# Kernel optimization log

Measured on AMD Instinct MI355X. Metric: run time of the kernel, lower is better.

The kernel has to match this reference:

```python
import jax, jax.numpy as jnp
import numpy as np


def setup_inputs() -> dict:
    key = jax.random.key(0)
    ks = jax.random.split(key, 8)
    B, T, U = 4, 400, 80
    De, Dd, V = 512, 512, 1024
    F = De + Dd  # in_features = 1024
    s = lambda k, shape: jax.random.normal(k, shape, dtype=jnp.float32) * 0.05
    return {
        "encoder_output": jax.random.normal(ks[0], (B, T, De), dtype=jnp.float32),
        "decoder_output": jax.random.normal(ks[1], (B, U, Dd), dtype=jnp.float32),
        "W_enc": s(ks[2], (F, De)),
        "b_enc": s(ks[3], (F,)),
        "W_dec": s(ks[4], (F, Dd)),
        "b_dec": s(ks[5], (F,)),
        "W_fc": s(ks[6], (V, F)),
        "b_fc": s(ks[7], (V,)),
    }


def reference(encoder_output, decoder_output, W_enc, b_enc, W_dec, b_dec, W_fc, b_fc):
    # fc_enc / fc_dec projections: (B,T,F) and (B,U,F)
    enc = jnp.einsum("btd,fd->btf", encoder_output, W_enc) + b_enc
    dec = jnp.einsum("bud,fd->buf", decoder_output, W_dec) + b_dec
    # broadcast-add -> (B,T,U,F)
    combined = enc[:, :, None, :] + dec[:, None, :, :]
    # fc: tanh then linear -> (B,T,U,V)
    vocab_logits = jnp.einsum("btuf,vf->btuv", jnp.tanh(combined), W_fc) + b_fc
    # HAT branch: blank prob via sigmoid of logit 0
    blk_logit = vocab_logits[..., :1]
    log_blk = jax.nn.log_sigmoid(blk_logit)          # log(sigmoid)
    log_not_blk = jax.nn.log_sigmoid(-blk_logit)     # log(1 - sigmoid)
    vocab_log_probs = log_not_blk + jax.nn.log_softmax(vocab_logits[..., 1:], axis=-1)
    return jnp.concatenate([log_blk, vocab_log_probs], axis=-1)
```

## Files before the change

### kernel.cpp

```cpp
#include <hip/hip_runtime.h>
#include <hip/hip_bf16.h>
#include <cstdint>
#include <cstddef>

typedef short bf16x8 __attribute__((ext_vector_type(8)));
typedef float f32x4 __attribute__((ext_vector_type(4)));

static __device__ __forceinline__ unsigned short f2bf(float f) {
    union { float f; uint32_t u; } c; c.f = f;
    uint32_t r = c.u + 0x7FFFu + ((c.u >> 16) & 1u);
    return (unsigned short)(r >> 16);
}

static __device__ __forceinline__ float fast_tanh(float x) {
    float e = __expf(2.0f * x);
    return 1.0f - 2.0f / (e + 1.0f);
}

static __device__ __forceinline__ float softplus_f(float x) {
    return fmaxf(x, 0.0f) + log1pf(__expf(-fabsf(x)));
}

__global__ __launch_bounds__(256) void k_convert(
    const float* __restrict__ s0, const float* __restrict__ s1,
    const float* __restrict__ s2, const float* __restrict__ s3,
    const float* __restrict__ s4,
    unsigned short* __restrict__ d0, unsigned short* __restrict__ d1,
    unsigned short* __restrict__ d2, unsigned short* __restrict__ d3,
    unsigned short* __restrict__ d4,
    int n0, int n1, int n2, int n3, int n4)
{
    int i = blockIdx.x * 256 + threadIdx.x;
    int c0 = n0 >> 2, c1 = c0 + (n1 >> 2), c2 = c1 + (n2 >> 2),
        c3 = c2 + (n3 >> 2), c4 = c3 + (n4 >> 2);
    if (i >= c4) return;
    const float* s; unsigned short* d; int j;
    if (i < c0)      { s = s0; d = d0; j = i; }
    else if (i < c1) { s = s1; d = d1; j = i - c0; }
    else if (i < c2) { s = s2; d = d2; j = i - c1; }
    else if (i < c3) { s = s3; d = d3; j = i - c2; }
    else             { s = s4; d = d4; j = i - c3; }
    float4 v = reinterpret_cast<const float4*>(s)[j];
    ushort4 o;
    o.x = f2bf(v.x); o.y = f2bf(v.y); o.z = f2bf(v.z); o.w = f2bf(v.w);
    reinterpret_cast<ushort4*>(d)[j] = o;
}

__global__ __launch_bounds__(256) void k_proj(
    const unsigned short* __restrict__ A,
    const unsigned short* __restrict__ W,
    const float* __restrict__ bias,
    float* __restrict__ out)
{
    __shared__ unsigned short As[32 * 512];
    const int tid = threadIdx.x;
    const int m0 = blockIdx.x * 32;
    const int c0 = blockIdx.y * 128;
    {
        int row = tid >> 3;
        const unsigned short* src = A + (size_t)(m0 + row) * 512;
        unsigned int base = row * 1024;
        unsigned int sw = (row & 7) << 4;
        #pragma unroll
        for (int c = 0; c < 8; ++c) {
            int col = (tid & 7) * 8 + c * 64;
            bf16x8 v = *reinterpret_cast<const bf16x8*>(src + col);
            *reinterpret_cast<bf16x8*>(
                reinterpret_cast<char*>(As) + ((base + col * 2) ^ sw)) = v;
        }
    }
    __syncthreads();
    const int w = tid >> 6, l = tid & 63;
    const int lr = l & 15, lkb = (l >> 4) * 8;
    f32x4 acc[2][2] = {};
    const int colbase = c0 + w * 32;
    const unsigned short* Wb = W + (size_t)(colbase + lr) * 512 + lkb;
    const unsigned int sw = (lr & 7) << 4;
    for (int ks = 0; ks < 16; ++ks) {
        unsigned int kb = (ks * 32 + lkb) * 2;
        bf16x8 a0 = *reinterpret_cast<const bf16x8*>(
            reinterpret_cast<const char*>(As) + ((lr * 1024 + kb) ^ sw));
        bf16x8 a1 = *reinterpret_cast<const bf16x8*>(
            reinterpret_cast<const char*>(As) + (((16 + lr) * 1024 + kb) ^ sw));
        #pragma unroll
        for (int nf = 0; nf < 2; ++nf) {
            bf16x8 b = *reinterpret_cast<const bf16x8*>(Wb + nf * 16 * 512 + ks * 32);
            acc[0][nf] = __builtin_amdgcn_mfma_f32_16x16x32_bf16(a0, b, acc[0][nf], 0, 0, 0);
            acc[1][nf] = __builtin_amdgcn_mfma_f32_16x16x32_bf16(a1, b, acc[1][nf], 0, 0, 0);
        }
    }
    const int qr = (l >> 4) * 4;
    #pragma unroll
    for (int nf = 0; nf < 2; ++nf) {
        int col = colbase + nf * 16 + lr;
        float bv = bias[col];
        #pragma unroll
        for (int mf = 0; mf < 2; ++mf)
            #pragma unroll
            for (int r = 0; r < 4; ++r)
                out[(size_t)(m0 + mf * 16 + qr + r) * 1024 + col] = acc[mf][nf][r] + bv;
    }
}

__global__ __launch_bounds__(512, 2) void k_main(
    const float* __restrict__ enc,
    const float* __restrict__ dec,
    const unsigned short* __restrict__ Wfc,
    const float* __restrict__ bfc,
    float* __restrict__ out)
{
    extern __shared__ char smem[];
    char* As   = smem;
    float* red  = (float*)(smem + 131072);
    float* l0sh = (float*)(smem + 133120);

    const int tid = threadIdx.x;
    const int w = tid >> 6, l = tid & 63;
    const int lr = l & 15, q = l >> 4;
    const int r0 = blockIdx.x * 64;

    {
        int row = tid >> 3, kc = tid & 7;
        int m = r0 + row;
        int bt = m / 80;
        int u  = m - bt * 80;
        int b  = bt / 400;
        const float* ep = enc + (size_t)bt * 1024 + kc * 8;
        const float* dp = dec + (size_t)(b * 80 + u) * 1024 + kc * 8;
        unsigned base = row * 2048 + kc * 16;
        unsigned sw = (row & 7) << 4;
        #pragma unroll
        for (int c = 0; c < 16; ++c) {
            float4 e0 = *(const float4*)(ep + c * 64);
            float4 e1 = *(const float4*)(ep + c * 64 + 4);
            float4 f0 = *(const float4*)(dp + c * 64);
            float4 f1 = *(const float4*)(dp + c * 64 + 4);
            union { unsigned short h[8]; bf16x8 v; } pk;
            pk.h[0] = f2bf(fast_tanh(e0.x + f0.x));
            pk.h[1] = f2bf(fast_tanh(e0.y + f0.y));
            pk.h[2] = f2bf(fast_tanh(e0.z + f0.z));
            pk.h[3] = f2bf(fast_tanh(e0.w + f0.w));
            pk.h[4] = f2bf(fast_tanh(e1.x + f1.x));
            pk.h[5] = f2bf(fast_tanh(e1.y + f1.y));
            pk.h[6] = f2bf(fast_tanh(e1.z + f1.z));
            pk.h[7] = f2bf(fast_tanh(e1.w + f1.w));
            *(bf16x8*)(As + ((base + c * 128) ^ sw)) = pk.v;
        }
    }
    __syncthreads();

    const unsigned short* Wb = Wfc + (size_t)(w * 128 + lr) * 1024 + q * 8;
    const unsigned sw = (lr & 7) << 4;

    f32x4 acc[4][8] = {};
    bf16x8 B0[8], B1[8];

    #pragma unroll
    for (int nf = 0; nf < 8; ++nf)
        B0[nf] = *(const bf16x8*)(Wb + nf * 16384);
    #pragma unroll
    for (int nf = 0; nf < 8; ++nf)
        B1[nf] = *(const bf16x8*)(Wb + nf * 16384 + 32);

    #pragma unroll
    for (int kp = 0; kp < 16; ++kp) {
        const int ks0 = 2 * kp, ks1 = 2 * kp + 1;
        {
            bf16x8 a[4];
            #pragma unroll
            for (int mf = 0; mf < 4; ++mf)
                a[mf] = *(const bf16x8*)(As +
                    (((unsigned)(lr * 2048 + mf * 32768 + q * 16 + ks0 * 64)) ^ sw));
            #pragma unroll
            for (int nf = 0; nf < 8; ++nf) {
                #pragma unroll
                for (int mf = 0; mf < 4; ++mf)
                    acc[mf][nf] = __builtin_amdgcn_mfma_f32_16x16x32_bf16(
                        a[mf], B0[nf], acc[mf][nf], 0, 0, 0);
                if (ks0 + 2 < 32)
                    B0[nf] = *(const bf16x8*)(Wb + nf * 16384 + (ks0 + 2) * 32);
            }
        }
        {
            bf16x8 a[4];
            #pragma unroll
            for (int mf = 0; mf < 4; ++mf)
                a[mf] = *(const bf16x8*)(As +
                    (((unsigned)(lr * 2048 + mf * 32768 + q * 16 + ks1 * 64)) ^ sw));
            #pragma unroll
            for (int nf = 0; nf < 8; ++nf) {
                #pragma unroll
                for (int mf = 0; mf < 4; ++mf)
                    acc[mf][nf] = __builtin_amdgcn_mfma_f32_16x16x32_bf16(
                        a[mf], B1[nf], acc[mf][nf], 0, 0, 0);
                if (ks1 + 2 < 32)
                    B1[nf] = *(const bf16x8*)(Wb + nf * 16384 + (ks1 + 2) * 32);
            }
        }
    }

    #pragma unroll
    for (int nf = 0; nf < 8; ++nf) {
        float bv = bfc[w * 128 + nf * 16 + lr];
        #pragma unroll
        for (int mf = 0; mf < 4; ++mf)
            #pragma unroll
            for (int r = 0; r < 4; ++r)
                acc[mf][nf][r] += bv;
    }
    const bool excl = (w == 0 && lr == 0);
    if (excl) {
        #pragma unroll
        for (int mf = 0; mf < 4; ++mf)
            #pragma unroll
            for (int r = 0; r < 4; ++r)
                l0sh[mf * 16 + q * 4 + r] = acc[mf][0][r];
    }
    float Mrow[4][4];
    #pragma unroll
    for (int mf = 0; mf < 4; ++mf)
        #pragma unroll
        for (int r = 0; r < 4; ++r) {
            float m = -3.0e38f;
            #pragma unroll
            for (int nf = 0; nf < 8; ++nf)
                if (!(excl && nf == 0)) m = fmaxf(m, acc[mf][nf][r]);
            #pragma unroll
            for (int s = 1; s < 16; s <<= 1)
                m = fmaxf(m, __shfl_xor(m, s, 16));
            if (lr == 0) red[(mf * 16 + q * 4 + r) * 8 + w] = m;
        }
    __syncthreads();
    #pragma unroll
    for (int mf = 0; mf < 4; ++mf)
        #pragma unroll
        for (int r = 0; r < 4; ++r) {
            int row = mf * 16 + q * 4 + r;
            float m = red[row * 8 + 0];
            #pragma unroll
            for (int j = 1; j < 8; ++j) m = fmaxf(m, red[row * 8 + j]);
            Mrow[mf][r] = m;
        }
    __syncthreads();
    #pragma unroll
    for (int mf = 0; mf < 4; ++mf)
        #pragma unroll
        for (int r = 0; r < 4; ++r) {
            float s = 0.0f;
            #pragma unroll
            for (int nf = 0; nf < 8; ++nf)
                if (!(excl && nf == 0)) s += __expf(acc[mf][nf][r] - Mrow[mf][r]);
            #pragma unroll
            for (int sh = 1; sh < 16; sh <<= 1)
                s += __shfl_xor(s, sh, 16);
            if (lr == 0) red[(mf * 16 + q * 4 + r) * 8 + w] = s;
        }
    __syncthreads();
    #pragma unroll
    for (int mf = 0; mf < 4; ++mf)
        #pragma unroll
        for (int r = 0; r < 4; ++r) {
            int row = mf * 16 + q * 4 + r;
            float s = red[row * 8 + 0];
            #pragma unroll
            for (int j = 1; j < 8; ++j) s += red[row * 8 + j];
            float lse = Mrow[mf][r] + __logf(s);
            float l0 = l0sh[row];
            float lnb = -softplus_f(l0);
            float* op = out + (size_t)(r0 + row) * 1024;
            #pragma unroll
            for (int nf = 0; nf < 8; ++nf) {
                int col = w * 128 + nf * 16 + lr;
                float val = (col == 0) ? (-softplus_f(-l0))
                                       : (acc[mf][nf][r] - lse + lnb);
                op[col] = val;
            }
        }
}

extern "C" void kernel_launch(void* const* d_in, const int* in_sizes, int n_in,
                              void* d_out, int out_size, void* d_ws, size_t ws_size,
                              hipStream_t stream)
{
    const float* encoder = (const float*)d_in[0];
    const float* decoder = (const float*)d_in[1];
    const float* W_enc   = (const float*)d_in[2];
    const float* b_enc   = (const float*)d_in[3];
    const float* W_dec   = (const float*)d_in[4];
    const float* b_dec   = (const float*)d_in[5];
    const float* W_fc    = (const float*)d_in[6];
    const float* b_fc    = (const float*)d_in[7];
    float* out = (float*)d_out;

    char* ws = (char*)d_ws;
    float*          enc_f  = (float*)(ws);
    float*          dec_f  = (float*)(ws + 6553600);
    unsigned short* Wfc_h  = (unsigned short*)(ws + 7864320);
    unsigned short* Wenc_h = (unsigned short*)(ws + 9961472);
    unsigned short* Wdec_h = (unsigned short*)(ws + 11010048);
    unsigned short* encI_h = (unsigned short*)(ws + 12058624);
    unsigned short* decI_h = (unsigned short*)(ws + 13697024);

    const int nEnc = 4 * 400 * 512, nDec = 4 * 80 * 512;
    const int nWe = 1024 * 512, nWd = 1024 * 512, nWf = 1024 * 1024;
    const int totalF4 = (nEnc + nDec + nWe + nWd + nWf) >> 2;
    k_convert<<<(totalF4 + 255) / 256, 256, 0, stream>>>(
        encoder, decoder, W_enc, W_dec, W_fc,
        encI_h, decI_h, Wenc_h, Wdec_h, Wfc_h,
        nEnc, nDec, nWe, nWd, nWf);

    k_proj<<<dim3(1600 / 32, 8), 256, 0, stream>>>(encI_h, Wenc_h, b_enc, enc_f);
    k_proj<<<dim3(320 / 32, 8), 256, 0, stream>>>(decI_h, Wdec_h, b_dec, dec_f);

    const int SMEM_BYTES = 133376;
    hipFuncSetAttribute(reinterpret_cast<const void*>(k_main),
                        hipFuncAttributeMaxDynamicSharedMemorySize, SMEM_BYTES);
    k_main<<<2000, 512, SMEM_BYTES, stream>>>(enc_f, dec_f, Wfc_h, b_fc, out);
}
```

Baseline: 786.8 us.

## Use 128-row tiles with 1024 threads, splitting vocab and K into halves

```diff
diff --git a/kernel.cpp b/kernel.cpp
--- a/kernel.cpp
+++ b/kernel.cpp
@@ -11,12 +11,16 @@
     uint32_t r = c.u + 0x7FFFu + ((c.u >> 16) & 1u);
     return (unsigned short)(r >> 16);
 }
-
+static __device__ __forceinline__ float bf2f_lo(uint32_t w) {
+    union { uint32_t u; float f; } c; c.u = w << 16; return c.f;
+}
+static __device__ __forceinline__ float bf2f_hi(uint32_t w) {
+    union { uint32_t u; float f; } c; c.u = w & 0xffff0000u; return c.f;
+}
 static __device__ __forceinline__ float fast_tanh(float x) {
     float e = __expf(2.0f * x);
     return 1.0f - 2.0f / (e + 1.0f);
 }
-
 static __device__ __forceinline__ float softplus_f(float x) {
     return fmaxf(x, 0.0f) + log1pf(__expf(-fabsf(x)));
 }
@@ -102,7 +106,7 @@
     }
 }
 
-__global__ __launch_bounds__(512, 2) void k_main(
+__global__ __launch_bounds__(1024, 4) void k_main(
     const float* __restrict__ enc,
     const float* __restrict__ dec,
     const unsigned short* __restrict__ Wfc,
@@ -110,172 +114,234 @@
     float* __restrict__ out)
 {
     extern __shared__ char smem[];
-    char* As   = smem;
+    char*  As   = smem;
     float* red  = (float*)(smem + 131072);
-    float* l0sh = (float*)(smem + 133120);
+    float* Mc   = (float*)(smem + 135168);
+    float* fin  = (float*)(smem + 135680);
+    float* f0sh = (float*)(smem + 136192);
+    float* l0sh = (float*)(smem + 136704);
 
     const int tid = threadIdx.x;
     const int w = tid >> 6, l = tid & 63;
     const int lr = l & 15, q = l >> 4;
-    const int r0 = blockIdx.x * 64;
-
+    const int wm = w >> 3, wn = w & 7;
+
+    const int bid = (int)blockIdx.x;
+    const int sbid = (bid & 7) * 125 + (bid >> 3);
+    const int r0 = sbid * 128;
+
+    const int arow = tid >> 3, akc = tid & 7;
+    const float *ep, *dp;
     {
-        int row = tid >> 3, kc = tid & 7;
-        int m = r0 + row;
+        int m = r0 + arow;
         int bt = m / 80;
-        int u  = m - bt * 80;
-        int b  = bt / 400;
-        const float* ep = enc + (size_t)bt * 1024 + kc * 8;
-        const float* dp = dec + (size_t)(b * 80 + u) * 1024 + kc * 8;
-        unsigned base = row * 2048 + kc * 16;
-        unsigned sw = (row & 7) << 4;
-        #pragma unroll
-        for (int c = 0; c < 16; ++c) {
-            float4 e0 = *(const float4*)(ep + c * 64);
-            float4 e1 = *(const float4*)(ep + c * 64 + 4);
-            float4 f0 = *(const float4*)(dp + c * 64);
-            float4 f1 = *(const float4*)(dp + c * 64 + 4);
-            union { unsigned short h[8]; bf16x8 v; } pk;
-            pk.h[0] = f2bf(fast_tanh(e0.x + f0.x));
-            pk.h[1] = f2bf(fast_tanh(e0.y + f0.y));
-            pk.h[2] = f2bf(fast_tanh(e0.z + f0.z));
-            pk.h[3] = f2bf(fast_tanh(e0.w + f0.w));
-            pk.h[4] = f2bf(fast_tanh(e1.x + f1.x));
-            pk.h[5] = f2bf(fast_tanh(e1.y + f1.y));
-            pk.h[6] = f2bf(fast_tanh(e1.z + f1.z));
-            pk.h[7] = f2bf(fast_tanh(e1.w + f1.w));
-            *(bf16x8*)(As + ((base + c * 128) ^ sw)) = pk.v;
+        int u = m - bt * 80;
+        int b = bt / 400;
+        ep = enc + (size_t)bt * 1024 + akc * 8;
+        dp = dec + (size_t)(b * 80 + u) * 1024 + akc * 8;
+    }
+    const unsigned awbase = (unsigned)(arow * 1024 + akc * 16);
+    const unsigned awkey  = (unsigned)((arow & 7) << 4);
+
+    const unsigned abase = (unsigned)((wm * 64 + lr) * 1024 + q * 16);
+    const unsigned akey  = (unsigned)((lr & 7) << 4);
+
+    char* stash = (char*)(out + (size_t)r0 * 1024 + 512) + w * 8192 + l * 16;
+
+    #pragma unroll
+    for (int vp = 0; vp < 2; ++vp) {
+        const unsigned short* Wv =
+            Wfc + (size_t)(vp * 512 + wn * 64 + lr) * 1024 + q * 8;
+        f32x4 acc[4][4] = {};
+        bf16x8 Bp0[4], Bp1[4];
+        #pragma unroll
+        for (int nf = 0; nf < 4; ++nf) Bp0[nf] = *(const bf16x8*)(Wv + nf * 16384);
+        #pragma unroll
+        for (int nf = 0; nf < 4; ++nf) Bp1[nf] = *(const bf16x8*)(Wv + nf * 16384 + 32);
+
+        #pragma unroll
+        for (int kh = 0; kh < 2; ++kh) {
+            __syncthreads();
+            {
+                const float* eph = ep + kh * 512;
+                const float* dph = dp + kh * 512;
+                #pragma unroll
+                for (int c = 0; c < 8; ++c) {
+                    float4 e0 = *(const float4*)(eph + c * 64);
+                    float4 e1 = *(const float4*)(eph + c * 64 + 4);
+                    float4 f0 = *(const float4*)(dph + c * 64);
+                    float4 f1 = *(const float4*)(dph + c * 64 + 4);
+                    union { unsigned short h[8]; bf16x8 v; } pk;
+                    pk.h[0] = f2bf(fast_tanh(e0.x + f0.x));
+                    pk.h[1] = f2bf(fast_tanh(e0.y + f0.y));
+                    pk.h[2] = f2bf(fast_tanh(e0.z + f0.z));
+                    pk.h[3] = f2bf(fast_tanh(e0.w + f0.w));
+                    pk.h[4] = f2bf(fast_tanh(e1.x + f1.x));
+                    pk.h[5] = f2bf(fast_tanh(e1.y + f1.y));
+                    pk.h[6] = f2bf(fast_tanh(e1.z + f1.z));
+                    pk.h[7] = f2bf(fast_tanh(e1.w + f1.w));
+                    *(bf16x8*)(As + ((awbase + c * 128) ^ awkey)) = pk.v;
+                }
+            }
+            __syncthreads();
+            #pragma unroll
+            for (int kp = 0; kp < 8; ++kp) {
+                {
+                    const int ks = kp * 2, gks = kh * 16 + ks;
+                    bf16x8 a[4];
+                    unsigned ao = (abase + ks * 64) ^ akey;
+                    #pragma unroll
+                    for (int mf = 0; mf < 4; ++mf)
+                        a[mf] = *(const bf16x8*)(As + ao + mf * 16384);
+                    #pragma unroll
+                    for (int nf = 0; nf < 4; ++nf) {
+                        #pragma unroll
+                        for (int mf = 0; mf < 4; ++mf)
+                            acc[mf][nf] = __builtin_amdgcn_mfma_f32_16x16x32_bf16(
+                                a[mf], Bp0[nf], acc[mf][nf], 0, 0, 0);
+                        if (gks + 2 < 32)
+                            Bp0[nf] = *(const bf16x8*)(Wv + nf * 16384 + (gks + 2) * 32);
+                    }
+                }
+                {
+                    const int ks = kp * 2 + 1, gks = kh * 16 + ks;
+                    bf16x8 a[4];
+                    unsigned ao = (abase + ks * 64) ^ akey;
+                    #pragma unroll
+                    for (int mf = 0; mf < 4; ++mf)
+                        a[mf] = *(const bf16x8*)(As + ao + mf * 16384);
+                    #pragma unroll
+                    for (int nf = 0; nf < 4; ++nf) {
+                        #pragma unroll
+                        for (int mf = 0; mf < 4; ++mf)
+                            acc[mf][nf] = __builtin_amdgcn_mfma_f32_16x16x32_bf16(
+                                a[mf], Bp1[nf], acc[mf][nf], 0, 0, 0);
+                        if (gks + 2 < 32)
+                            Bp1[nf] = *(const bf16x8*)(Wv + nf * 16384 + (gks + 2) * 32);
+                    }
+                }
+            }
         }
-    }
-    __syncthreads();
-
-    const unsigned short* Wb = Wfc + (size_t)(w * 128 + lr) * 1024 + q * 8;
-    const unsigned sw = (lr & 7) << 4;
-
-    f32x4 acc[4][8] = {};
-    bf16x8 B0[8], B1[8];
-
-    #pragma unroll
-    for (int nf = 0; nf < 8; ++nf)
-        B0[nf] = *(const bf16x8*)(Wb + nf * 16384);
-    #pragma unroll
-    for (int nf = 0; nf < 8; ++nf)
-        B1[nf] = *(const bf16x8*)(Wb + nf * 16384 + 32);
-
-    #pragma unroll
-    for (int kp = 0; kp < 16; ++kp) {
-        const int ks0 = 2 * kp, ks1 = 2 * kp + 1;
-        {
-            bf16x8 a[4];
+
+        if (vp == 0) {
+            #pragma unroll
+            for (int nf = 0; nf < 4; ++nf) {
+                float bv = bfc[wn * 64 + nf * 16 + lr];
+                #pragma unroll
+                for (int mf = 0; mf < 4; ++mf)
+                    #pragma unroll
+                    for (int r = 0; r < 4; ++r)
+                        acc[mf][nf][r] += bv;
+            }
+            uint32_t wds[32];
             #pragma unroll
             for (int mf = 0; mf < 4; ++mf)
-                a[mf] = *(const bf16x8*)(As +
-                    (((unsigned)(lr * 2048 + mf * 32768 + q * 16 + ks0 * 64)) ^ sw));
-            #pragma unroll
-            for (int nf = 0; nf < 8; ++nf) {
+                #pragma unroll
+                for (int nf = 0; nf < 4; ++nf) {
+                    wds[mf * 8 + nf * 2 + 0] =
+                        (uint32_t)f2bf(acc[mf][nf][0]) | ((uint32_t)f2bf(acc[mf][nf][1]) << 16);
+                    wds[mf * 8 + nf * 2 + 1] =
+                        (uint32_t)f2bf(acc[mf][nf][2]) | ((uint32_t)f2bf(acc[mf][nf][3]) << 16);
+                }
+            #pragma unroll
+            for (int i = 0; i < 8; ++i) {
+                uint4 v = { wds[4*i], wds[4*i+1], wds[4*i+2], wds[4*i+3] };
+                *(uint4*)(stash + i * 1024) = v;
+            }
+        } else {
+            uint32_t wds[32];
+            #pragma unroll
+            for (int i = 0; i < 8; ++i) {
+                uint4 v = *(const uint4*)(stash + i * 1024);
+                wds[4*i] = v.x; wds[4*i+1] = v.y; wds[4*i+2] = v.z; wds[4*i+3] = v.w;
+            }
+            #define SV(mf, nf, r) ((r & 1) ? bf2f_hi(wds[(mf)*8+(nf)*2+((r)>>1)]) \
+                                           : bf2f_lo(wds[(mf)*8+(nf)*2+((r)>>1)]))
+            #pragma unroll
+            for (int nf = 0; nf < 4; ++nf) {
+                float bv = bfc[512 + wn * 64 + nf * 16 + lr];
                 #pragma unroll
                 for (int mf = 0; mf < 4; ++mf)
-                    acc[mf][nf] = __builtin_amdgcn_mfma_f32_16x16x32_bf16(
-                        a[mf], B0[nf], acc[mf][nf], 0, 0, 0);
-                if (ks0 + 2 < 32)
-                    B0[nf] = *(const bf16x8*)(Wb + nf * 16384 + (ks0 + 2) * 32);
-            }
+                    #pragma unroll
+                    for (int r = 0; r < 4; ++r)
+                        acc[mf][nf][r] += bv;
+            }
+            const bool excl = (wn == 0 && lr == 0);
+            if (excl) {
+                #pragma unroll
+                for (int mf = 0; mf < 4; ++mf)
+                    #pragma unroll
+                    for (int r = 0; r < 4; ++r)
+                        l0sh[wm * 64 + mf * 16 + q * 4 + r] = SV(mf, 0, r);
+            }
+            #pragma unroll
+            for (int mf = 0; mf < 4; ++mf)
+                #pragma unroll
+                for (int r = 0; r < 4; ++r) {
+                    float m = -3.0e38f;
+                    #pragma unroll
+                    for (int nf = 0; nf < 4; ++nf) {
+                        if (!(excl && nf == 0)) m = fmaxf(m, SV(mf, nf, r));
+                        m = fmaxf(m, acc[mf][nf][r]);
+                    }
+                    #pragma unroll
+                    for (int s = 1; s < 16; s <<= 1)
+                        m = fmaxf(m, __shfl_xor(m, s, 16));
+                    if (lr == 0) red[(wm * 64 + mf * 16 + q * 4 + r) * 8 + wn] = m;
+                }
+            __syncthreads();
+            if (tid < 128) {
+                float m = red[tid * 8];
+                #pragma unroll
+                for (int j = 1; j < 8; ++j) m = fmaxf(m, red[tid * 8 + j]);
+                Mc[tid] = m;
+            }
+            __syncthreads();
+            #pragma unroll
+            for (int mf = 0; mf < 4; ++mf)
+                #pragma unroll
+                for (int r = 0; r < 4; ++r) {
+                    int rl = wm * 64 + mf * 16 + q * 4 + r;
+                    float M = Mc[rl];
+                    float s = 0.0f;
+                    #pragma unroll
+                    for (int nf = 0; nf < 4; ++nf) {
+                        if (!(excl && nf == 0)) s += __expf(SV(mf, nf, r) - M);
+                        s += __expf(acc[mf][nf][r] - M);
+                    }
+                    #pragma unroll
+                    for (int sh = 1; sh < 16; sh <<= 1)
+                        s += __shfl_xor(s, sh, 16);
+                    if (lr == 0) red[rl * 8 + wn] = s;
+                }
+            __syncthreads();
+            if (tid < 128) {
+                float s = red[tid * 8];
+                #pragma unroll
+                for (int j = 1; j < 8; ++j) s += red[tid * 8 + j];
+                float lse = Mc[tid] + __logf(s);
+                float l0 = l0sh[tid];
+                fin[tid]  = -lse - softplus_f(l0);
+                f0sh[tid] = -softplus_f(-l0);
+            }
+            __syncthreads();
+            #pragma unroll
+            for (int mf = 0; mf < 4; ++mf)
+                #pragma unroll
+                for (int r = 0; r < 4; ++r) {
+                    int rl = wm * 64 + mf * 16 + q * 4 + r;
+                    float fv = fin[rl];
+                    float* op = out + (size_t)(r0 + rl) * 1024;
+                    #pragma unroll
+                    for (int nf = 0; nf < 4; ++nf) {
+                        int col = wn * 64 + nf * 16 + lr;
+                        op[col] = (col == 0) ? f0sh[rl] : SV(mf, nf, r) + fv;
+                        op[512 + col] = acc[mf][nf][r] + fv;
+                    }
+                }
+            #undef SV
         }
-        {
-            bf16x8 a[4];
-            #pragma unroll
-            for (int mf = 0; mf < 4; ++mf)
-                a[mf] = *(const bf16x8*)(As +
-                    (((unsigned)(lr * 2048 + mf * 32768 + q * 16 + ks1 * 64)) ^ sw));
-            #pragma unroll
-            for (int nf = 0; nf < 8; ++nf) {
-                #pragma unroll
-                for (int mf = 0; mf < 4; ++mf)
-                    acc[mf][nf] = __builtin_amdgcn_mfma_f32_16x16x32_bf16(
-                        a[mf], B1[nf], acc[mf][nf], 0, 0, 0);
-                if (ks1 + 2 < 32)
-                    B1[nf] = *(const bf16x8*)(Wb + nf * 16384 + (ks1 + 2) * 32);
-            }
-        }
-    }
-
-    #pragma unroll
-    for (int nf = 0; nf < 8; ++nf) {
-        float bv = bfc[w * 128 + nf * 16 + lr];
-        #pragma unroll
-        for (int mf = 0; mf < 4; ++mf)
-            #pragma unroll
-            for (int r = 0; r < 4; ++r)
-                acc[mf][nf][r] += bv;
-    }
-    const bool excl = (w == 0 && lr == 0);
-    if (excl) {
-        #pragma unroll
-        for (int mf = 0; mf < 4; ++mf)
-            #pragma unroll
-            for (int r = 0; r < 4; ++r)
-                l0sh[mf * 16 + q * 4 + r] = acc[mf][0][r];
-    }
-    float Mrow[4][4];
-    #pragma unroll
-    for (int mf = 0; mf < 4; ++mf)
-        #pragma unroll
-        for (int r = 0; r < 4; ++r) {
-            float m = -3.0e38f;
-            #pragma unroll
-            for (int nf = 0; nf < 8; ++nf)
-                if (!(excl && nf == 0)) m = fmaxf(m, acc[mf][nf][r]);
-            #pragma unroll
-            for (int s = 1; s < 16; s <<= 1)
-                m = fmaxf(m, __shfl_xor(m, s, 16));
-            if (lr == 0) red[(mf * 16 + q * 4 + r) * 8 + w] = m;
-        }
-    __syncthreads();
-    #pragma unroll
-    for (int mf = 0; mf < 4; ++mf)
-        #pragma unroll
-        for (int r = 0; r < 4; ++r) {
-            int row = mf * 16 + q * 4 + r;
-            float m = red[row * 8 + 0];
-            #pragma unroll
-            for (int j = 1; j < 8; ++j) m = fmaxf(m, red[row * 8 + j]);
-            Mrow[mf][r] = m;
-        }
-    __syncthreads();
-    #pragma unroll
-    for (int mf = 0; mf < 4; ++mf)
-        #pragma unroll
-        for (int r = 0; r < 4; ++r) {
-            float s = 0.0f;
-            #pragma unroll
-            for (int nf = 0; nf < 8; ++nf)
-                if (!(excl && nf == 0)) s += __expf(acc[mf][nf][r] - Mrow[mf][r]);
-            #pragma unroll
-            for (int sh = 1; sh < 16; sh <<= 1)
-                s += __shfl_xor(s, sh, 16);
-            if (lr == 0) red[(mf * 16 + q * 4 + r) * 8 + w] = s;
-        }
-    __syncthreads();
-    #pragma unroll
-    for (int mf = 0; mf < 4; ++mf)
-        #pragma unroll
-        for (int r = 0; r < 4; ++r) {
-            int row = mf * 16 + q * 4 + r;
-            float s = red[row * 8 + 0];
-            #pragma unroll
-            for (int j = 1; j < 8; ++j) s += red[row * 8 + j];
-            float lse = Mrow[mf][r] + __logf(s);
-            float l0 = l0sh[row];
-            float lnb = -softplus_f(l0);
-            float* op = out + (size_t)(r0 + row) * 1024;
-            #pragma unroll
-            for (int nf = 0; nf < 8; ++nf) {
-                int col = w * 128 + nf * 16 + lr;
-                float val = (col == 0) ? (-softplus_f(-l0))
-                                       : (acc[mf][nf][r] - lse + lnb);
-                op[col] = val;
-            }
-        }
+    }
 }
 
 extern "C" void kernel_launch(void* const* d_in, const int* in_sizes, int n_in,
@@ -312,8 +378,8 @@
     k_proj<<<dim3(1600 / 32, 8), 256, 0, stream>>>(encI_h, Wenc_h, b_enc, enc_f);
     k_proj<<<dim3(320 / 32, 8), 256, 0, stream>>>(decI_h, Wdec_h, b_dec, dec_f);
 
-    const int SMEM_BYTES = 133376;
+    const int SMEM_BYTES = 137216;
     hipFuncSetAttribute(reinterpret_cast<const void*>(k_main),
                         hipFuncAttributeMaxDynamicSharedMemorySize, SMEM_BYTES);
-    k_main<<<2000, 512, SMEM_BYTES, stream>>>(enc_f, dec_f, Wfc_h, b_fc, out);
-}
+    k_main<<<1000, 1024, SMEM_BYTES, stream>>>(enc_f, dec_f, Wfc_h, b_fc, out);
+}
```

After: 1.898 ms. +141.3%, slower.
